# Optimization experiments

Hardware: AMD Instinct MI355X
Metric: run time of the kernel (lower is better)

Reference implementation:

```python
import jax, jax.numpy as jnp
import numpy as np

N, FEATURES, CODES, PAGES = 32768, 768, 64, 8192
BETA = 0.25


def _normalise(x):
    return x / jnp.linalg.norm(x, axis=-1, keepdims=True)


def setup_inputs() -> dict:
    key = jax.random.key(0)
    k_z, k_wi, k_wo, k_cb = jax.random.split(key, 4)
    return {
        "z": jax.random.normal(k_z, (N, FEATURES), dtype=jnp.float32),
        "w_in": jax.random.normal(k_wi, (CODES, FEATURES), dtype=jnp.float32) * 0.02,
        "b_in": jnp.zeros((CODES,), dtype=jnp.float32),
        "w_out": jax.random.normal(k_wo, (FEATURES, CODES), dtype=jnp.float32) * 0.02,
        "b_out": jnp.zeros((FEATURES,), dtype=jnp.float32),
        "codebook": jax.random.normal(k_cb, (PAGES, CODES), dtype=jnp.float32),
    }


def reference(z, w_in, b_in, w_out, b_out, codebook):
    sg = jax.lax.stop_gradient
    # project + L2-normalise samples and codes
    zq = _normalise(z @ w_in.T + b_in)          # [n, codes]
    cn = _normalise(codebook)                   # [pages, codes]
    # squared euclidean distance without materialising [n, pages, codes]:
    # ||z||^2 + ||c||^2 - 2 z c^T
    d = (
        jnp.sum(zq * zq, axis=-1, keepdims=True)
        + jnp.sum(cn * cn, axis=-1)[None, :]
        - 2.0 * (zq @ cn.T)
    )                                           # [n, pages]
    idxes = jnp.argmin(d, axis=-1)              # [n]
    codes = _normalise(codebook[idxes])         # lookup then normalise, as in source
    loss = BETA * jnp.mean((sg(zq) - codes) ** 2) + jnp.mean((zq - sg(codes)) ** 2)
    codes = zq + sg(codes - zq)                 # straight-through
    out = codes @ w_out.T + b_out               # [n, features]
    return out, loss, idxes
```

## Files before the change

### kernel.cpp

```cpp
#include <hip/hip_runtime.h>

#define N 32768
#define F 768
#define C 64
#define P 8192
#define TAU 1e-3f

typedef __attribute__((ext_vector_type(8))) short short8;
typedef __attribute__((ext_vector_type(4))) float f32x4;

#define WS_CNT    0
#define WS_CC     (WS_CNT + C*P)
#define WS_ZQT    (WS_CC + P)
#define WS_CODEST (WS_ZQT + C*N)
#define WS_IDX    (WS_CODEST + C*N)
#define WS_QN     (WS_IDX + N)
#define WS_ACC    (WS_QN + 1)
#define WS_QLIST  (WS_ACC + 1)
#define WS_CNH    ((WS_QLIST + N + 3) & ~3)
#define WS_CNL    (WS_CNH + (C*P)/2)
#define WS_ZQH    (WS_CNL + (C*P)/2)
#define WS_ZQL    (WS_ZQH + (C*N)/2)
#define WS_D12    (WS_ZQL + (C*N)/2)
#define WS_WOH    (WS_D12 + 16*N)
#define WS_WOL    (WS_WOH + (F*C)/2)

#define OUT_LOSS_OFF (N*F)
#define OUT_IDX_OFF  (N*F + 1)

__device__ inline unsigned short f2bf(float x) {
    union { float f; unsigned u; } v; v.f = x;
    unsigned r = v.u + 0x7fffu + ((v.u >> 16) & 1u);
    return (unsigned short)(r >> 16);
}
__device__ inline float bf2f(unsigned short b) {
    union { unsigned u; float f; } v; v.u = ((unsigned)b) << 16;
    return v.f;
}

__global__ __launch_bounds__(256) void k1_norm_codebook(
    const float* __restrict__ cb, float* __restrict__ cnT, float* __restrict__ cc,
    unsigned short* __restrict__ cnh, unsigned short* __restrict__ cnl) {
    int p = blockIdx.x * 256 + threadIdx.x;
    const float4* cb4 = (const float4*)(cb + (size_t)p * C);
    float4 v[16];
    float ss = 0.f;
#pragma unroll
    for (int i = 0; i < 16; ++i) {
        v[i] = cb4[i];
        ss += v[i].x * v[i].x + v[i].y * v[i].y + v[i].z * v[i].z + v[i].w * v[i].w;
    }
    float nrm = sqrtf(ss);
    float s2 = 0.f;
    unsigned short hb[64], lb[64];
#pragma unroll
    for (int i = 0; i < 16; ++i) {
        float c4[4] = {v[i].x / nrm, v[i].y / nrm, v[i].z / nrm, v[i].w / nrm};
#pragma unroll
        for (int j = 0; j < 4; ++j) {
            cnT[(size_t)(i * 4 + j) * P + p] = c4[j];
            s2 += c4[j] * c4[j];
            unsigned short h = f2bf(c4[j]);
            hb[i * 4 + j] = h;
            lb[i * 4 + j] = f2bf(c4[j] - bf2f(h));
        }
    }
    cc[p] = s2;
#pragma unroll
    for (int i = 0; i < 8; ++i) {
        uint4 hv, lv;
        hv.x = (unsigned)hb[i*8+0] | ((unsigned)hb[i*8+1] << 16);
        hv.y = (unsigned)hb[i*8+2] | ((unsigned)hb[i*8+3] << 16);
        hv.z = (unsigned)hb[i*8+4] | ((unsigned)hb[i*8+5] << 16);
        hv.w = (unsigned)hb[i*8+6] | ((unsigned)hb[i*8+7] << 16);
        lv.x = (unsigned)lb[i*8+0] | ((unsigned)lb[i*8+1] << 16);
        lv.y = (unsigned)lb[i*8+2] | ((unsigned)lb[i*8+3] << 16);
        lv.z = (unsigned)lb[i*8+4] | ((unsigned)lb[i*8+5] << 16);
        lv.w = (unsigned)lb[i*8+6] | ((unsigned)lb[i*8+7] << 16);
        *(uint4*)&cnh[(size_t)p * 64 + i * 8] = hv;
        *(uint4*)&cnl[(size_t)p * 64 + i * 8] = lv;
    }
}

__global__ __launch_bounds__(256) void k2_project(
    const float* __restrict__ z, const float* __restrict__ w_in, const float* __restrict__ b_in,
    float* __restrict__ zqT, unsigned short* __restrict__ zqh, unsigned short* __restrict__ zql) {
    __shared__ float zrow[64 * 33];
    __shared__ float wrow[64 * 32];
    __shared__ float red[64 * 9];
    int tid = threadIdx.x;
    int tr = tid & 31;
    int tc = tid >> 5;
    int rb = blockIdx.x * 64;

    float y[2][8];
#pragma unroll
    for (int i = 0; i < 2; ++i)
#pragma unroll
        for (int j = 0; j < 8; ++j) y[i][j] = 0.f;

    for (int kt = 0; kt < F; kt += 32) {
        __syncthreads();
        for (int i = tid; i < 64 * 32; i += 256) {
            int r = i >> 5, k = i & 31;
            zrow[r * 33 + k] = z[(size_t)(rb + r) * F + kt + k];
        }
        for (int i = tid; i < 64 * 32; i += 256) {
            int c = i >> 5, k = i & 31;
            wrow[c * 32 + k] = w_in[(size_t)c * F + kt + k];
        }
        __syncthreads();
#pragma unroll
        for (int k4 = 0; k4 < 8; ++k4) {
            float zs[2][4];
#pragma unroll
            for (int i = 0; i < 2; ++i)
#pragma unroll
                for (int kk = 0; kk < 4; ++kk)
                    zs[i][kk] = zrow[(tr + 32 * i) * 33 + k4 * 4 + kk];
#pragma unroll
            for (int j = 0; j < 8; ++j) {
                float4 wv = *(const float4*)&wrow[(tc * 8 + j) * 32 + k4 * 4];
#pragma unroll
                for (int i = 0; i < 2; ++i)
                    y[i][j] = fmaf(zs[i][3], wv.w,
                              fmaf(zs[i][2], wv.z,
                              fmaf(zs[i][1], wv.y,
                              fmaf(zs[i][0], wv.x, y[i][j]))));
            }
        }
    }
#pragma unroll
    for (int j = 0; j < 8; ++j) {
        float b = b_in[tc * 8 + j];
#pragma unroll
        for (int i = 0; i < 2; ++i) y[i][j] += b;
    }
    __syncthreads();
#pragma unroll
    for (int i = 0; i < 2; ++i) {
        float s = 0.f;
#pragma unroll
        for (int j = 0; j < 8; ++j) s += y[i][j] * y[i][j];
        red[(tr + 32 * i) * 9 + tc] = s;
    }
    __syncthreads();
    float nrm[2];
#pragma unroll
    for (int i = 0; i < 2; ++i) {
        float t = 0.f;
#pragma unroll
        for (int t8 = 0; t8 < 8; ++t8) t += red[(tr + 32 * i) * 9 + t8];
        nrm[i] = sqrtf(t);
    }
    float q[2][8];
#pragma unroll
    for (int i = 0; i < 2; ++i)
#pragma unroll
        for (int j = 0; j < 8; ++j) q[i][j] = y[i][j] / nrm[i];
#pragma unroll
    for (int j = 0; j < 8; ++j) {
        int c = tc * 8 + j;
#pragma unroll
        for (int i = 0; i < 2; ++i)
            zqT[(size_t)c * N + rb + tr + 32 * i] = q[i][j];
    }
#pragma unroll
    for (int i = 0; i < 2; ++i) {
        unsigned short h[8], l[8];
#pragma unroll
        for (int j = 0; j < 8; ++j) {
            h[j] = f2bf(q[i][j]);
            l[j] = f2bf(q[i][j] - bf2f(h[j]));
        }
        uint4 hv, lv;
        hv.x = (unsigned)h[0] | ((unsigned)h[1] << 16);
        hv.y = (unsigned)h[2] | ((unsigned)h[3] << 16);
        hv.z = (unsigned)h[4] | ((unsigned)h[5] << 16);
        hv.w = (unsigned)h[6] | ((unsigned)h[7] << 16);
        lv.x = (unsigned)l[0] | ((unsigned)l[1] << 16);
        lv.y = (unsigned)l[2] | ((unsigned)l[3] << 16);
        lv.z = (unsigned)l[4] | ((unsigned)l[5] << 16);
        lv.w = (unsigned)l[6] | ((unsigned)l[7] << 16);
        size_t ro = (size_t)(rb + tr + 32 * i) * 64 + tc * 8;
        *(uint4*)&zqh[ro] = hv;
        *(uint4*)&zql[ro] = lv;
    }
}

__global__ __launch_bounds__(256, 4) void k3_argmin_mfma(
    const unsigned short* __restrict__ zqh, const unsigned short* __restrict__ zql,
    const unsigned short* __restrict__ cnh, const unsigned short* __restrict__ cnl,
    float4* __restrict__ d12) {
    __shared__ unsigned short lfrag[8 * 4 * 64 * 8];
    int tid = threadIdx.x;
    int w = tid >> 6, lane = tid & 63;
    int col = lane & 15, quad = lane >> 4;
    int rb = (blockIdx.x & 255) * 128;
    int ph = blockIdx.x >> 8;
    int wrow = rb + w * 32;
    int p0 = ph * (P / 4);

    short8 ah[2][2], al[2][2];
#pragma unroll
    for (int mm = 0; mm < 2; ++mm)
#pragma unroll
        for (int kf = 0; kf < 2; ++kf) {
            size_t off = (size_t)(wrow + mm * 16 + col) * 64 + kf * 32 + quad * 8;
            ah[mm][kf] = *(const short8*)&zqh[off];
            al[mm][kf] = *(const short8*)&zql[off];
        }

    float s1[8], s2[8]; int i1[8];
#pragma unroll
    for (int r = 0; r < 8; ++r) { s1[r] = -3.4e38f; s2[r] = -3.4e38f; i1[r] = 0; }

    int sq = (tid >> 4) & 3, scol = tid & 15, sf = w;
    const unsigned short* ssrc = (sf & 2) ? cnl : cnh;
    int skf = sf & 1;

    for (int pt = p0; pt < p0 + P / 4; pt += 128) {
        __syncthreads();
#pragma unroll
        for (int nt = 0; nt < 8; ++nt) {
            int p = pt + nt * 16 + scol;
            uint4 dv = *(const uint4*)&ssrc[(size_t)p * 64 + skf * 32 + sq * 8];
            *(uint4*)&lfrag[((nt * 4 + sf) * 64 + (tid & 63)) * 8] = dv;
        }
        __syncthreads();
#pragma unroll 2
        for (int nt = 0; nt < 8; ++nt) {
            short8 bh0 = *(const short8*)&lfrag[((nt * 4 + 0) * 64 + lane) * 8];
            short8 bh1 = *(const short8*)&lfrag[((nt * 4 + 1) * 64 + lane) * 8];
            short8 bl0 = *(const short8*)&lfrag[((nt * 4 + 2) * 64 + lane) * 8];
            short8 bl1 = *(const short8*)&lfrag[((nt * 4 + 3) * 64 + lane) * 8];
            int p = pt + nt * 16 + col;
#pragma unroll
            for (int mm = 0; mm < 2; ++mm) {
                f32x4 acc = {0.f, 0.f, 0.f, 0.f};
                acc = __builtin_amdgcn_mfma_f32_16x16x32_bf16(ah[mm][0], bh0, acc, 0, 0, 0);
                acc = __builtin_amdgcn_mfma_f32_16x16x32_bf16(ah[mm][1], bh1, acc, 0, 0, 0);
                acc = __builtin_amdgcn_mfma_f32_16x16x32_bf16(ah[mm][0], bl0, acc, 0, 0, 0);
                acc = __builtin_amdgcn_mfma_f32_16x16x32_bf16(ah[mm][1], bl1, acc, 0, 0, 0);
                acc = __builtin_amdgcn_mfma_f32_16x16x32_bf16(al[mm][0], bh0, acc, 0, 0, 0);
                acc = __builtin_amdgcn_mfma_f32_16x16x32_bf16(al[mm][1], bh1, acc, 0, 0, 0);
#pragma unroll
                for (int s = 0; s < 4; ++s) {
                    float sv = acc[s];
                    int r = mm * 4 + s;
                    bool gt = sv > s1[r];
                    i1[r] = gt ? p : i1[r];
                    s2[r] = fmaxf(s2[r], fminf(s1[r], sv));
                    s1[r] = fmaxf(s1[r], sv);
                }
            }
        }
    }
#pragma unroll
    for (int r = 0; r < 8; ++r) {
        float a1v = s1[r], a2v = s2[r]; int ai = i1[r];
#pragma unroll
        for (int m = 1; m <= 8; m <<= 1) {
            float b1 = __shfl_xor(a1v, m); int bi = __shfl_xor(ai, m);
            float b2 = __shfl_xor(a2v, m);
            float n1 = fmaxf(a1v, b1);
            a2v = fmaxf(fminf(a1v, b1), fmaxf(a2v, b2));
            ai = (b1 > a1v) ? bi : ai;
            a1v = n1;
        }
        if (col == 0) {
            int row = wrow + (r >> 2) * 16 + quad * 4 + (r & 3);
            d12[ph * N + row] = make_float4(a1v, a2v, __int_as_float(ai), 0.f);
        }
    }
}

__global__ __launch_bounds__(256) void k3m_merge(
    const float4* __restrict__ d12, int* __restrict__ idx_ws, float* __restrict__ idx_out,
    int* __restrict__ qn, int* __restrict__ qlist) {
    int row = blockIdx.x * 256 + threadIdx.x;
    float4 a = d12[row];
    float m1 = a.x, m2 = a.y; int i1 = __float_as_int(a.z);
#pragma unroll
    for (int ph = 1; ph < 4; ++ph) {
        float4 b = d12[ph * N + row];
        m2 = fmaxf(fminf(m1, b.x), fmaxf(m2, b.y));
        if (b.x > m1) { i1 = __float_as_int(b.z); m1 = b.x; }
    }
    idx_ws[row] = i1;
    idx_out[row] = (float)i1;
    if (m1 - m2 < 0.5f * TAU + 2e-6f) {
        int qi = atomicAdd(qn, 1);
        qlist[qi] = row;
    }
}

__global__ __launch_bounds__(256) void k3_recheck(
    const float* __restrict__ zqT, const float* __restrict__ cnT,
    const float* __restrict__ cc, const int* __restrict__ qn,
    const int* __restrict__ qlist, int* __restrict__ idx_ws, float* __restrict__ idx_out) {
    __shared__ float zrow[64];
    __shared__ float bv[4];
    __shared__ int   bi4[4];
    int tid = threadIdx.x, w = tid >> 6, lane = tid & 63;
    int nq = qn[0];
    for (int e = blockIdx.x; e < nq; e += gridDim.x) {
        int row = qlist[e];
        __syncthreads();
        if (tid < 64) zrow[tid] = zqT[(size_t)tid * N + row];
        __syncthreads();
        float best = 3.4e38f; int bp = 0;
        for (int pb = w * 2048; pb < (w + 1) * 2048; pb += 64) {
            int p = pb + lane;
            float a0 = 0.f, a1 = 0.f, a2 = 0.f, a3 = 0.f;
#pragma unroll
            for (int k = 0; k < 64; k += 4) {
                a0 = fmaf(zrow[k + 0], cnT[(size_t)(k + 0) * P + p], a0);
                a1 = fmaf(zrow[k + 1], cnT[(size_t)(k + 1) * P + p], a1);
                a2 = fmaf(zrow[k + 2], cnT[(size_t)(k + 2) * P + p], a2);
                a3 = fmaf(zrow[k + 3], cnT[(size_t)(k + 3) * P + p], a3);
            }
            float d = fmaf((a0 + a1) + (a2 + a3), -2.0f, cc[p]);
            if (d < best) { best = d; bp = p; }
        }
#pragma unroll
        for (int m = 1; m < 64; m <<= 1) {
            float ob = __shfl_xor(best, m); int op = __shfl_xor(bp, m);
            if (ob < best || (ob == best && op < bp)) { best = ob; bp = op; }
        }
        if (lane == 0) { bv[w] = best; bi4[w] = bp; }
        __syncthreads();
        if (tid == 0) {
            float b = bv[0]; int pi = bi4[0];
#pragma unroll
            for (int ww = 1; ww < 4; ++ww)
                if (bv[ww] < b || (bv[ww] == b && bi4[ww] < pi)) { b = bv[ww]; pi = bi4[ww]; }
            idx_ws[row] = pi; idx_out[row] = (float)pi;
        }
    }
}

__global__ __launch_bounds__(256) void k3b_gather_loss(
    const float* __restrict__ cnT, const int* __restrict__ idx,
    const float* __restrict__ zqT, float* __restrict__ acc) {
    float s = 0.f;
    for (size_t i = (size_t)blockIdx.x * 256 + threadIdx.x; i < (size_t)C * N;
         i += (size_t)gridDim.x * 256) {
        int k = (int)(i >> 15);
        int r = (int)(i & (N - 1));
        float d = zqT[i] - cnT[(size_t)k * P + idx[r]];
        s = fmaf(d, d, s);
    }
#pragma unroll
    for (int off = 32; off > 0; off >>= 1) s += __shfl_xor(s, off);
    __shared__ float wsum[4];
    int lane = threadIdx.x & 63, wv = threadIdx.x >> 6;
    if (lane == 0) wsum[wv] = s;
    __syncthreads();
    if (threadIdx.x == 0) atomicAdd(acc, wsum[0] + wsum[1] + wsum[2] + wsum[3]);
}

__global__ __launch_bounds__(256) void k4_prep(
    const float* __restrict__ w_out, unsigned short* __restrict__ woh,
    unsigned short* __restrict__ wol) {
    int i = blockIdx.x * 256 + threadIdx.x;
    float v = w_out[i];
    unsigned short h = f2bf(v);
    woh[i] = h;
    wol[i] = f2bf(v - bf2f(h));
}

__global__ __launch_bounds__(256) void k4_out_mfma(
    const unsigned short* __restrict__ cnh, const unsigned short* __restrict__ cnl,
    const unsigned short* __restrict__ woh, const unsigned short* __restrict__ wol,
    const int* __restrict__ idx, const float* __restrict__ b_out, float* __restrict__ out) {
    int tid = threadIdx.x;
    int w = tid >> 6, lane = tid & 63;
    int col = lane & 15, quad = lane >> 4;
    int rb = (blockIdx.x >> 2) * 64;
    int fb = (blockIdx.x & 3) * 192;
    int wrow = rb + w * 16;

    int pg = idx[wrow + col];
    short8 ah[2], al[2];
#pragma unroll
    for (int kf = 0; kf < 2; ++kf) {
        size_t off = (size_t)pg * 64 + kf * 32 + quad * 8;
        ah[kf] = *(const short8*)&cnh[off];
        al[kf] = *(const short8*)&cnl[off];
    }

    for (int ft = 0; ft < 12; ++ft) {
        int f0 = fb + ft * 16;
        size_t bo = (size_t)(f0 + col) * 64 + quad * 8;
        short8 bh0 = *(const short8*)&woh[bo];
        short8 bh1 = *(const short8*)&woh[bo + 32];
        short8 bl0 = *(const short8*)&wol[bo];
        short8 bl1 = *(const short8*)&wol[bo + 32];
        f32x4 acc = {0.f, 0.f, 0.f, 0.f};
        acc = __builtin_amdgcn_mfma_f32_16x16x32_bf16(ah[0], bh0, acc, 0, 0, 0);
        acc = __builtin_amdgcn_mfma_f32_16x16x32_bf16(ah[1], bh1, acc, 0, 0, 0);
        acc = __builtin_amdgcn_mfma_f32_16x16x32_bf16(ah[0], bl0, acc, 0, 0, 0);
        acc = __builtin_amdgcn_mfma_f32_16x16x32_bf16(ah[1], bl1, acc, 0, 0, 0);
        acc = __builtin_amdgcn_mfma_f32_16x16x32_bf16(al[0], bh0, acc, 0, 0, 0);
        acc = __builtin_amdgcn_mfma_f32_16x16x32_bf16(al[1], bh1, acc, 0, 0, 0);
        float bv = b_out[f0 + col];
#pragma unroll
        for (int s = 0; s < 4; ++s)
            out[(size_t)(wrow + quad * 4 + s) * F + f0 + col] = acc[s] + bv;
    }
}

__global__ void k6_finalize(const float* __restrict__ acc, float* __restrict__ loss_out) {
    float m = acc[0] / (float)(C * N);
    loss_out[0] = 0.25f * m + m;
}

extern "C" void kernel_launch(void* const* d_in, const int* in_sizes, int n_in,
                              void* d_out, int out_size, void* d_ws, size_t ws_size,
                              hipStream_t stream) {
    const float* z      = (const float*)d_in[0];
    const float* w_in   = (const float*)d_in[1];
    const float* b_in   = (const float*)d_in[2];
    const float* w_out  = (const float*)d_in[3];
    const float* b_out  = (const float*)d_in[4];
    const float* cb     = (const float*)d_in[5];
    float* out = (float*)d_out;
    float* ws  = (float*)d_ws;

    unsigned short* cnh = (unsigned short*)(ws + WS_CNH);
    unsigned short* cnl = (unsigned short*)(ws + WS_CNL);
    unsigned short* zqh = (unsigned short*)(ws + WS_ZQH);
    unsigned short* zql = (unsigned short*)(ws + WS_ZQL);
    unsigned short* woh = (unsigned short*)(ws + WS_WOH);
    unsigned short* wol = (unsigned short*)(ws + WS_WOL);

    hipMemsetAsync(ws + WS_QN, 0, 2 * sizeof(float), stream);
    k1_norm_codebook<<<P / 256, 256, 0, stream>>>(cb, ws + WS_CNT, ws + WS_CC, cnh, cnl);
    k4_prep<<<F * C / 256, 256, 0, stream>>>(w_out, woh, wol);
    k2_project<<<N / 64, 256, 0, stream>>>(z, w_in, b_in, ws + WS_ZQT, zqh, zql);
    k3_argmin_mfma<<<1024, 256, 0, stream>>>(zqh, zql, cnh, cnl, (float4*)(ws + WS_D12));
    k3m_merge<<<N / 256, 256, 0, stream>>>((const float4*)(ws + WS_D12),
                                           (int*)(ws + WS_IDX), out + OUT_IDX_OFF,
                                           (int*)(ws + WS_QN), (int*)(ws + WS_QLIST));
    k3_recheck<<<512, 256, 0, stream>>>(ws + WS_ZQT, ws + WS_CNT, ws + WS_CC,
                                        (const int*)(ws + WS_QN), (const int*)(ws + WS_QLIST),
                                        (int*)(ws + WS_IDX), out + OUT_IDX_OFF);
    k3b_gather_loss<<<2048, 256, 0, stream>>>(ws + WS_CNT, (const int*)(ws + WS_IDX),
                                              ws + WS_ZQT, ws + WS_ACC);
    k4_out_mfma<<<2048, 256, 0, stream>>>(cnh, cnl, woh, wol, (const int*)(ws + WS_IDX),
                                          b_out, out);
    k6_finalize<<<1, 1, 0, stream>>>(ws + WS_ACC, out + OUT_LOSS_OFF);
}
```

Baseline: 614.1 us.

## Move input projection to bf16x3 split MFMA with pre-split weights

The scalar FP32 projection kernel z @ w_in^T is replaced by an MFMA kernel. It splits z on the fly, and w_in in a new prep kernel, into three bf16 parts and accumulates six cross-product MFMAs to emulate FP32 precision. Normalisation now uses wave shuffles, and outputs are staged through LDS so the zq bf16 and transposed writes are coalesced. This targets the FP32 ALU cost of the 32768x768x64 GEMM. In exchange it adds one prep launch, reuses the otherwise idle CODEST workspace region for the split weights, and gives a small precision difference that could affect argmin near-ties.

Result: faster. 529.2 us (-13.8%).

```diff
diff --git a/kernel.cpp b/kernel.cpp
--- a/kernel.cpp
+++ b/kernel.cpp
@@ -13,6 +13,9 @@
 #define WS_CC     (WS_CNT + C*P)
 #define WS_ZQT    (WS_CC + P)
 #define WS_CODEST (WS_ZQT + C*N)
+#define WS_WIH    WS_CODEST
+#define WS_WIM    (WS_WIH + (C*F)/2)
+#define WS_WIL    (WS_WIM + (C*F)/2)
 #define WS_IDX    (WS_CODEST + C*N)
 #define WS_QN     (WS_IDX + N)
 #define WS_ACC    (WS_QN + 1)
@@ -36,6 +39,27 @@
 __device__ inline float bf2f(unsigned short b) {
     union { unsigned u; float f; } v; v.u = ((unsigned)b) << 16;
     return v.f;
+}
+
+union U32S8 { unsigned u[4]; short8 s; };
+
+__device__ inline void split3x8(const float* xp, short8& h, short8& m, short8& l) {
+    U32S8 hh, mm, ll;
+#pragma unroll
+    for (int i = 0; i < 4; ++i) {
+        float xa = xp[2 * i], xb = xp[2 * i + 1];
+        unsigned ha = __float_as_uint(xa) & 0xffff0000u;
+        unsigned hb = __float_as_uint(xb) & 0xffff0000u;
+        hh.u[i] = (ha >> 16) | hb;
+        float ra = xa - __uint_as_float(ha), rb = xb - __uint_as_float(hb);
+        unsigned ma = __float_as_uint(ra) & 0xffff0000u;
+        unsigned mb = __float_as_uint(rb) & 0xffff0000u;
+        mm.u[i] = (ma >> 16) | mb;
+        float sa = ra - __uint_as_float(ma), sb = rb - __uint_as_float(mb);
+        ll.u[i] = ((__float_as_uint(sa) & 0xffff0000u) >> 16) |
+                  (__float_as_uint(sb) & 0xffff0000u);
+    }
+    h = hh.s; m = mm.s; l = ll.s;
 }
 
 __global__ __launch_bounds__(256) void k1_norm_codebook(
@@ -82,109 +106,113 @@
     }
 }
 
-__global__ __launch_bounds__(256) void k2_project(
-    const float* __restrict__ z, const float* __restrict__ w_in, const float* __restrict__ b_in,
-    float* __restrict__ zqT, unsigned short* __restrict__ zqh, unsigned short* __restrict__ zql) {
-    __shared__ float zrow[64 * 33];
-    __shared__ float wrow[64 * 32];
-    __shared__ float red[64 * 9];
-    int tid = threadIdx.x;
-    int tr = tid & 31;
-    int tc = tid >> 5;
-    int rb = blockIdx.x * 64;
-
-    float y[2][8];
-#pragma unroll
-    for (int i = 0; i < 2; ++i)
-#pragma unroll
-        for (int j = 0; j < 8; ++j) y[i][j] = 0.f;
-
-    for (int kt = 0; kt < F; kt += 32) {
-        __syncthreads();
-        for (int i = tid; i < 64 * 32; i += 256) {
-            int r = i >> 5, k = i & 31;
-            zrow[r * 33 + k] = z[(size_t)(rb + r) * F + kt + k];
-        }
-        for (int i = tid; i < 64 * 32; i += 256) {
-            int c = i >> 5, k = i & 31;
-            wrow[c * 32 + k] = w_in[(size_t)c * F + kt + k];
-        }
-        __syncthreads();
-#pragma unroll
-        for (int k4 = 0; k4 < 8; ++k4) {
-            float zs[2][4];
-#pragma unroll
-            for (int i = 0; i < 2; ++i)
-#pragma unroll
-                for (int kk = 0; kk < 4; ++kk)
-                    zs[i][kk] = zrow[(tr + 32 * i) * 33 + k4 * 4 + kk];
-#pragma unroll
-            for (int j = 0; j < 8; ++j) {
-                float4 wv = *(const float4*)&wrow[(tc * 8 + j) * 32 + k4 * 4];
-#pragma unroll
-                for (int i = 0; i < 2; ++i)
-                    y[i][j] = fmaf(zs[i][3], wv.w,
-                              fmaf(zs[i][2], wv.z,
-                              fmaf(zs[i][1], wv.y,
-                              fmaf(zs[i][0], wv.x, y[i][j]))));
-            }
-        }
-    }
-#pragma unroll
-    for (int j = 0; j < 8; ++j) {
-        float b = b_in[tc * 8 + j];
-#pragma unroll
-        for (int i = 0; i < 2; ++i) y[i][j] += b;
-    }
+__global__ __launch_bounds__(256) void k2_prep(
+    const float* __restrict__ w_in, unsigned short* __restrict__ wih,
+    unsigned short* __restrict__ wim, unsigned short* __restrict__ wil) {
+    int i = blockIdx.x * 256 + threadIdx.x;
+    float x = w_in[i];
+    unsigned hu = __float_as_uint(x) & 0xffff0000u;
+    float r1 = x - __uint_as_float(hu);
+    unsigned mu = __float_as_uint(r1) & 0xffff0000u;
+    float r2 = r1 - __uint_as_float(mu);
+    wih[i] = (unsigned short)(hu >> 16);
+    wim[i] = (unsigned short)(mu >> 16);
+    wil[i] = f2bf(r2);
+}
+
+__global__ __launch_bounds__(64) void k2_project_mfma(
+    const float* __restrict__ z,
+    const unsigned short* __restrict__ wih, const unsigned short* __restrict__ wim,
+    const unsigned short* __restrict__ wil, const float* __restrict__ b_in,
+    float* __restrict__ zqT, unsigned short* __restrict__ zqh,
+    unsigned short* __restrict__ zql) {
+    __shared__ float lq[16 * 65];
+    int lane = threadIdx.x;
+    int col = lane & 15, quad = lane >> 4;
+    int wrow = blockIdx.x * 16;
+
+    f32x4 acc[4];
+#pragma unroll
+    for (int nt = 0; nt < 4; ++nt) acc[nt] = (f32x4){0.f, 0.f, 0.f, 0.f};
+
+    const float* zrow = z + (size_t)(wrow + col) * F + quad * 8;
+    size_t bbase[4];
+#pragma unroll
+    for (int nt = 0; nt < 4; ++nt) bbase[nt] = (size_t)(nt * 16 + col) * F + quad * 8;
+
+#pragma unroll 2
+    for (int kt = 0; kt < F / 32; ++kt) {
+        float xz[8];
+        *(float4*)&xz[0] = *(const float4*)&zrow[kt * 32];
+        *(float4*)&xz[4] = *(const float4*)&zrow[kt * 32 + 4];
+        short8 ah, am, al;
+        split3x8(xz, ah, am, al);
+#pragma unroll
+        for (int nt = 0; nt < 4; ++nt) {
+            size_t bo = bbase[nt] + kt * 32;
+            short8 bh = *(const short8*)&wih[bo];
+            short8 bm = *(const short8*)&wim[bo];
+            short8 bl = *(const short8*)&wil[bo];
+            acc[nt] = __builtin_amdgcn_mfma_f32_16x16x32_bf16(ah, bh, acc[nt], 0, 0, 0);
+            acc[nt] = __builtin_amdgcn_mfma_f32_16x16x32_bf16(ah, bm, acc[nt], 0, 0, 0);
+            acc[nt] = __builtin_amdgcn_mfma_f32_16x16x32_bf16(am, bh, acc[nt], 0, 0, 0);
+            acc[nt] = __builtin_amdgcn_mfma_f32_16x16x32_bf16(ah, bl, acc[nt], 0, 0, 0);
+            acc[nt] = __builtin_amdgcn_mfma_f32_16x16x32_bf16(al, bh, acc[nt], 0, 0, 0);
+            acc[nt] = __builtin_amdgcn_mfma_f32_16x16x32_bf16(am, bm, acc[nt], 0, 0, 0);
+        }
+    }
+    float y[4][4];
+#pragma unroll
+    for (int nt = 0; nt < 4; ++nt) {
+        float bv = b_in[nt * 16 + col];
+#pragma unroll
+        for (int s = 0; s < 4; ++s) y[nt][s] = acc[nt][s] + bv;
+    }
+#pragma unroll
+    for (int s = 0; s < 4; ++s) {
+        float ssum = 0.f;
+#pragma unroll
+        for (int nt = 0; nt < 4; ++nt) ssum += y[nt][s] * y[nt][s];
+#pragma unroll
+        for (int m = 1; m <= 8; m <<= 1) ssum += __shfl_xor(ssum, m);
+        float nrm = sqrtf(ssum);
+#pragma unroll
+        for (int nt = 0; nt < 4; ++nt) y[nt][s] /= nrm;
+    }
+#pragma unroll
+    for (int nt = 0; nt < 4; ++nt)
+#pragma unroll
+        for (int s = 0; s < 4; ++s)
+            lq[(quad * 4 + s) * 65 + nt * 16 + col] = y[nt][s];
     __syncthreads();
-#pragma unroll
-    for (int i = 0; i < 2; ++i) {
-        float s = 0.f;
-#pragma unroll
-        for (int j = 0; j < 8; ++j) s += y[i][j] * y[i][j];
-        red[(tr + 32 * i) * 9 + tc] = s;
-    }
-    __syncthreads();
-    float nrm[2];
-#pragma unroll
-    for (int i = 0; i < 2; ++i) {
-        float t = 0.f;
-#pragma unroll
-        for (int t8 = 0; t8 < 8; ++t8) t += red[(tr + 32 * i) * 9 + t8];
-        nrm[i] = sqrtf(t);
-    }
-    float q[2][8];
-#pragma unroll
-    for (int i = 0; i < 2; ++i)
-#pragma unroll
-        for (int j = 0; j < 8; ++j) q[i][j] = y[i][j] / nrm[i];
-#pragma unroll
-    for (int j = 0; j < 8; ++j) {
-        int c = tc * 8 + j;
-#pragma unroll
-        for (int i = 0; i < 2; ++i)
-            zqT[(size_t)c * N + rb + tr + 32 * i] = q[i][j];
-    }
-#pragma unroll
-    for (int i = 0; i < 2; ++i) {
-        unsigned short h[8], l[8];
-#pragma unroll
-        for (int j = 0; j < 8; ++j) {
-            h[j] = f2bf(q[i][j]);
-            l[j] = f2bf(q[i][j] - bf2f(h[j]));
-        }
-        uint4 hv, lv;
-        hv.x = (unsigned)h[0] | ((unsigned)h[1] << 16);
-        hv.y = (unsigned)h[2] | ((unsigned)h[3] << 16);
-        hv.z = (unsigned)h[4] | ((unsigned)h[5] << 16);
-        hv.w = (unsigned)h[6] | ((unsigned)h[7] << 16);
-        lv.x = (unsigned)l[0] | ((unsigned)l[1] << 16);
-        lv.y = (unsigned)l[2] | ((unsigned)l[3] << 16);
-        lv.z = (unsigned)l[4] | ((unsigned)l[5] << 16);
-        lv.w = (unsigned)l[6] | ((unsigned)l[7] << 16);
-        size_t ro = (size_t)(rb + tr + 32 * i) * 64 + tc * 8;
-        *(uint4*)&zqh[ro] = hv;
-        *(uint4*)&zql[ro] = lv;
+    {
+        int r = lane >> 2, part = lane & 3;
+        float v[16];
+#pragma unroll
+        for (int t = 0; t < 16; ++t) v[t] = lq[r * 65 + part * 16 + t];
+        unsigned hu[8], lu[8];
+#pragma unroll
+        for (int k = 0; k < 8; ++k) {
+            unsigned short h0 = f2bf(v[2 * k]), h1 = f2bf(v[2 * k + 1]);
+            unsigned short l0 = f2bf(v[2 * k] - bf2f(h0));
+            unsigned short l1 = f2bf(v[2 * k + 1] - bf2f(h1));
+            hu[k] = (unsigned)h0 | ((unsigned)h1 << 16);
+            lu[k] = (unsigned)l0 | ((unsigned)l1 << 16);
+        }
+        size_t ro = (size_t)(wrow + r) * 64 + part * 16;
+        *(uint4*)&zqh[ro] = make_uint4(hu[0], hu[1], hu[2], hu[3]);
+        *(uint4*)&zqh[ro + 8] = make_uint4(hu[4], hu[5], hu[6], hu[7]);
+        *(uint4*)&zql[ro] = make_uint4(lu[0], lu[1], lu[2], lu[3]);
+        *(uint4*)&zql[ro + 8] = make_uint4(lu[4], lu[5], lu[6], lu[7]);
+    }
+    {
+        float t[16];
+#pragma unroll
+        for (int r = 0; r < 16; ++r) t[r] = lq[r * 65 + lane];
+        float* dst = &zqT[(size_t)lane * N + wrow];
+#pragma unroll
+        for (int g = 0; g < 4; ++g)
+            *(float4*)&dst[g * 4] = make_float4(t[4 * g], t[4 * g + 1], t[4 * g + 2], t[4 * g + 3]);
     }
 }
 
@@ -434,11 +462,16 @@
     unsigned short* zql = (unsigned short*)(ws + WS_ZQL);
     unsigned short* woh = (unsigned short*)(ws + WS_WOH);
     unsigned short* wol = (unsigned short*)(ws + WS_WOL);
+    unsigned short* wih = (unsigned short*)(ws + WS_WIH);
+    unsigned short* wim = (unsigned short*)(ws + WS_WIM);
+    unsigned short* wil = (unsigned short*)(ws + WS_WIL);
 
     hipMemsetAsync(ws + WS_QN, 0, 2 * sizeof(float), stream);
     k1_norm_codebook<<<P / 256, 256, 0, stream>>>(cb, ws + WS_CNT, ws + WS_CC, cnh, cnl);
+    k2_prep<<<C * F / 256, 256, 0, stream>>>(w_in, wih, wim, wil);
     k4_prep<<<F * C / 256, 256, 0, stream>>>(w_out, woh, wol);
-    k2_project<<<N / 64, 256, 0, stream>>>(z, w_in, b_in, ws + WS_ZQT, zqh, zql);
+    k2_project_mfma<<<N / 16, 64, 0, stream>>>(z, wih, wim, wil, b_in,
+                                               ws + WS_ZQT, zqh, zql);
     k3_argmin_mfma<<<1024, 256, 0, stream>>>(zqh, zql, cnh, cnl, (float4*)(ws + WS_D12));
     k3m_merge<<<N / 256, 256, 0, stream>>>((const float4*)(ws + WS_D12),
                                            (int*)(ws + WS_IDX), out + OUT_IDX_OFF,
```
